# Kernel tuning notes

Measured on AMD Instinct MI355X. Metric: run time of the kernel, lower is better.

The kernel has to match this reference:

```python
import jax, jax.numpy as jnp
import numpy as np

D = 4          # simulated tensor-parallel devices (shard_axis size)
B, S = 2, 4096 # batch, seq_len
DIN_S = 512    # per-device input feature shard (full d_model = D*DIN_S = 2048)
DOUT_S = 2048  # per-device output feature shard (full d_out = D*DOUT_S = 8192)


def setup_inputs() -> dict:
    key = jax.random.key(0)
    kx, kw, kb = jax.random.split(key, 3)
    x = jax.random.normal(kx, (D, B, S, DIN_S), dtype=jnp.float32)
    # lecun_normal-style scale: std = 1/sqrt(fan_in) with fan_in = full input dim
    W = jax.random.normal(kw, (D, D, DIN_S, DOUT_S), dtype=jnp.float32) / np.sqrt(D * DIN_S)
    b = jax.random.normal(kb, (D, DOUT_S), dtype=jnp.float32) * 0.01
    return {"x": x, "W": W, "b": b}


def reference(x, W, b):
    # 'gather' TP strategy: device d gathers all input shards x_i and computes
    #   y_d = sum_i x_i @ W[d, i] + b[d]   (bias only added once, by shard idx==0)
    # x: [D, B, S, DIN_S], W: [D_out_dev, D_in_shard, DIN_S, DOUT_S], b: [D, DOUT_S]
    y = jnp.einsum('ibsk,diko->dbso', x, W)  # sum over gathered shards i and k
    return y + b[:, None, None, :]
```

## Files before the change

### kernel.cpp

```cpp
#include <hip/hip_runtime.h>
#include <hip/hip_bf16.h>

#define D_   4
#define M_   8192
#define K_   2048
#define N_   2048
#define DIN  512

typedef __attribute__((ext_vector_type(8))) short  short8v;
typedef __attribute__((ext_vector_type(4))) float  f32x4;

__device__ __forceinline__ unsigned short f2bf(float f) {
  union { float f; unsigned int u; } v; v.f = f;
  unsigned int u = v.u;
  return (unsigned short)((u + 0x7fffu + ((u >> 16) & 1u)) >> 16);
}

__global__ __launch_bounds__(256) void convert_x_kernel(const float* __restrict__ x,
                                                        unsigned short* __restrict__ A) {
  unsigned int tid = blockIdx.x * 256u + threadIdx.x;
  unsigned int kg  = tid & 63u;
  unsigned int i   = (tid >> 6) & 3u;
  unsigned int m   = tid >> 8;
  const float4* src = (const float4*)(x + (size_t)i * ((size_t)M_ * DIN)
                                        + (size_t)m * DIN + (size_t)kg * 8);
  float4 a = src[0];
  float4 b = src[1];
  uint4 pk;
  pk.x = (unsigned int)f2bf(a.x) | ((unsigned int)f2bf(a.y) << 16);
  pk.y = (unsigned int)f2bf(a.z) | ((unsigned int)f2bf(a.w) << 16);
  pk.z = (unsigned int)f2bf(b.x) | ((unsigned int)f2bf(b.y) << 16);
  pk.w = (unsigned int)f2bf(b.z) | ((unsigned int)f2bf(b.w) << 16);
  *(uint4*)(A + (size_t)tid * 8) = pk;
}

__global__ __launch_bounds__(256) void transpose_w_kernel(const float* __restrict__ W,
                                                          unsigned short* __restrict__ Wt) {
  __shared__ float tile[64][65];
  const int d  = blockIdx.z;
  const int k0 = blockIdx.x * 64;
  const int o0 = blockIdx.y * 64;
  const int t  = threadIdx.x;
  const float* src = W + (size_t)d * ((size_t)K_ * N_) + (size_t)k0 * N_ + o0;
  const int c4 = (t & 15) * 4;
  const int r  = t >> 4;
  #pragma unroll
  for (int j = 0; j < 64; j += 16) {
    float4 v = *(const float4*)(src + (size_t)(r + j) * N_ + c4);
    tile[r + j][c4 + 0] = v.x; tile[r + j][c4 + 1] = v.y;
    tile[r + j][c4 + 2] = v.z; tile[r + j][c4 + 3] = v.w;
  }
  __syncthreads();
  unsigned short* dst = Wt + (size_t)d * ((size_t)N_ * K_);
  const int kk = (t & 7) * 8;
  const int oo = t >> 3;
  #pragma unroll
  for (int p = 0; p < 64; p += 32) {
    const int o = oo + p;
    unsigned short tmp[8];
    #pragma unroll
    for (int i = 0; i < 8; i++) tmp[i] = f2bf(tile[kk + i][o]);
    *(uint4*)(dst + (size_t)(o0 + o) * K_ + k0 + kk) = *(uint4*)tmp;
  }
}

#define GLL16(gp, lp)                                                              \
  __builtin_amdgcn_global_load_lds(                                               \
      (const __attribute__((address_space(1))) void*)(gp),                        \
      (__attribute__((address_space(3))) void*)(lp), 16, 0, 0)

__global__ __launch_bounds__(256) void gemm_kernel(const unsigned short* __restrict__ A,
                                                   const unsigned short* __restrict__ Bt,
                                                   const float* __restrict__ bias,
                                                   float* __restrict__ C) {
  __shared__ unsigned short sA[128 * 64];
  __shared__ unsigned short sB[128 * 64];
  const int tid   = threadIdx.x;
  const int wave  = tid >> 6;
  const int lane  = tid & 63;
  const int d     = blockIdx.z;

  const int lin   = blockIdx.y * 16 + blockIdx.x;
  const int xcd   = lin & 7;
  const int t     = lin >> 3;
  const int tileN = (xcd * 2 + (t & 1)) * 128;
  const int tileM = (t >> 1) * 128;

  const int srow = lane >> 3;
  const int scol = ((lane & 7) ^ srow) * 8;
  const unsigned short* gA = A + (size_t)(tileM + wave * 32 + srow) * K_ + scol;
  const unsigned short* gB = Bt + (size_t)d * ((size_t)N_ * K_)
                                + (size_t)(tileN + wave * 32 + srow) * K_ + scol;
  unsigned short* lA = sA + (wave * 32) * 64;
  unsigned short* lB = sB + (wave * 32) * 64;

  const int wm   = (wave >> 1) * 64;
  const int wn   = (wave & 1) * 64;
  const int fr   = lane & 15;
  const int qw   = lane >> 4;
  const int fc0  = (qw ^ (fr & 7)) * 8;

  f32x4 acc[4][4];
  #pragma unroll
  for (int i = 0; i < 4; i++)
    #pragma unroll
    for (int j = 0; j < 4; j++)
      acc[i][j] = (f32x4){0.f, 0.f, 0.f, 0.f};

  for (int k0 = 0; k0 < K_; k0 += 64) {
    #pragma unroll
    for (int j = 0; j < 4; j++) {
      GLL16(gA + (size_t)j * 8 * K_ + k0, lA + j * 8 * 64);
      GLL16(gB + (size_t)j * 8 * K_ + k0, lB + j * 8 * 64);
    }
    __syncthreads();

    #pragma unroll
    for (int ks = 0; ks < 2; ks++) {
      const int fc = fc0 ^ (ks * 32);
      short8v af[4], bfv[4];
      #pragma unroll
      for (int mi = 0; mi < 4; mi++)
        af[mi] = *(const short8v*)(sA + (wm + mi * 16 + fr) * 64 + fc);
      #pragma unroll
      for (int ni = 0; ni < 4; ni++)
        bfv[ni] = *(const short8v*)(sB + (wn + ni * 16 + fr) * 64 + fc);
      #pragma unroll
      for (int mi = 0; mi < 4; mi++)
        #pragma unroll
        for (int ni = 0; ni < 4; ni++)
          acc[mi][ni] = __builtin_amdgcn_mfma_f32_16x16x32_bf16(af[mi], bfv[ni],
                                                                acc[mi][ni], 0, 0, 0);
    }
    __syncthreads();
  }

  float* Cd       = C + (size_t)d * ((size_t)M_ * N_);
  const float* bd = bias + d * N_;
  #pragma unroll
  for (int ni = 0; ni < 4; ni++) {
    const int col  = tileN + wn + ni * 16 + fr;
    const float bv = bd[col];
    #pragma unroll
    for (int mi = 0; mi < 4; mi++) {
      const int row0 = tileM + wm + mi * 16 + qw * 4;
      #pragma unroll
      for (int r = 0; r < 4; r++)
        Cd[(size_t)(row0 + r) * N_ + col] = acc[mi][ni][r] + bv;
    }
  }
}

__global__ void naive_kernel(const float* __restrict__ x, const float* __restrict__ W,
                             const float* __restrict__ bias, float* __restrict__ y) {
  long idx = (long)blockIdx.x * blockDim.x + threadIdx.x;
  if (idx >= (long)D_ * M_ * N_) return;
  int  n = (int)(idx % N_);
  long t = idx / N_;
  int  m = (int)(t % M_);
  int  d = (int)(t / M_);
  float acc = bias[d * N_ + n];
  const float* wd = W + (size_t)d * ((size_t)K_ * N_);
  for (int i = 0; i < D_; i++) {
    const float* xr = x + (size_t)i * ((size_t)M_ * DIN) + (size_t)m * DIN;
    const float* wr = wd + (size_t)i * ((size_t)DIN * N_) + n;
    #pragma unroll 4
    for (int k = 0; k < DIN; k++) acc += xr[k] * wr[(size_t)k * N_];
  }
  y[idx] = acc;
}

extern "C" void kernel_launch(void* const* d_in, const int* in_sizes, int n_in,
                              void* d_out, int out_size, void* d_ws, size_t ws_size,
                              hipStream_t stream) {
  const float* x    = (const float*)d_in[0];
  const float* W    = (const float*)d_in[1];
  const float* bias = (const float*)d_in[2];
  float* out        = (float*)d_out;

  const size_t a_elems  = (size_t)M_ * K_;
  const size_t wt_elems = (size_t)D_ * N_ * K_;
  const size_t need     = (a_elems + wt_elems) * sizeof(unsigned short);

  if (ws_size >= need) {
    unsigned short* Abf = (unsigned short*)d_ws;
    unsigned short* Wt  = Abf + a_elems;

    convert_x_kernel<<<(M_ * K_ / 8) / 256, 256, 0, stream>>>(x, Abf);

    dim3 tgrid(K_ / 64, N_ / 64, D_);
    transpose_w_kernel<<<tgrid, 256, 0, stream>>>(W, Wt);

    dim3 ggrid(N_ / 128, M_ / 128, D_);
    gemm_kernel<<<ggrid, 256, 0, stream>>>(Abf, Wt, bias, out);
  } else {
    long total = (long)D_ * M_ * N_;
    naive_kernel<<<(unsigned int)((total + 255) / 256), 256, 0, stream>>>(x, W, bias, out);
  }
}
```

Before: 615.0 us.

## Use 256x256 GEMM tiles with 4-stage LDS pipeline and 512 threads

Restructures the bf16 GEMM to 256x256 block tiles with 8 waves, K-step 32, and a 4-deep ring of LDS buffers filled by direct global-to-LDS loads issued three tiles ahead. A single barrier per step with explicit vmcnt waits replaces the two-barrier load-then-compute loop, so memory latency can overlap MFMA work. It also raises MFMA priority, changes the tile-to-XCD mapping, and raises per-wave accumulator count. The cost is 128KB of LDS per block and more registers, which limits occupancy.

```diff
diff --git a/kernel.cpp b/kernel.cpp
--- a/kernel.cpp
+++ b/kernel.cpp
@@ -69,83 +69,103 @@
       (const __attribute__((address_space(1))) void*)(gp),                        \
       (__attribute__((address_space(3))) void*)(lp), 16, 0, 0)
 
-__global__ __launch_bounds__(256) void gemm_kernel(const unsigned short* __restrict__ A,
-                                                   const unsigned short* __restrict__ Bt,
-                                                   const float* __restrict__ bias,
-                                                   float* __restrict__ C) {
-  __shared__ unsigned short sA[128 * 64];
-  __shared__ unsigned short sB[128 * 64];
-  const int tid   = threadIdx.x;
-  const int wave  = tid >> 6;
-  const int lane  = tid & 63;
-  const int d     = blockIdx.z;
-
-  const int lin   = blockIdx.y * 16 + blockIdx.x;
-  const int xcd   = lin & 7;
-  const int t     = lin >> 3;
-  const int tileN = (xcd * 2 + (t & 1)) * 128;
-  const int tileM = (t >> 1) * 128;
-
-  const int srow = lane >> 3;
-  const int scol = ((lane & 7) ^ srow) * 8;
-  const unsigned short* gA = A + (size_t)(tileM + wave * 32 + srow) * K_ + scol;
-  const unsigned short* gB = Bt + (size_t)d * ((size_t)N_ * K_)
-                                + (size_t)(tileN + wave * 32 + srow) * K_ + scol;
-  unsigned short* lA = sA + (wave * 32) * 64;
-  unsigned short* lB = sB + (wave * 32) * 64;
-
-  const int wm   = (wave >> 1) * 64;
-  const int wn   = (wave & 1) * 64;
-  const int fr   = lane & 15;
-  const int qw   = lane >> 4;
-  const int fc0  = (qw ^ (fr & 7)) * 8;
-
-  f32x4 acc[4][4];
-  #pragma unroll
-  for (int i = 0; i < 4; i++)
+#define NT_ 64
+
+__global__ __launch_bounds__(512, 2) void gemm_kernel(const unsigned short* __restrict__ A,
+                                                      const unsigned short* __restrict__ Bt,
+                                                      const float* __restrict__ bias,
+                                                      float* __restrict__ C) {
+  __shared__ __align__(16) unsigned short sA[4 * 8192];
+  __shared__ __align__(16) unsigned short sB[4 * 8192];
+  const int tid  = threadIdx.x;
+  const int w    = tid >> 6;
+  const int lane = tid & 63;
+  const int d    = blockIdx.z;
+
+  const int lin     = blockIdx.y * 8 + blockIdx.x;
+  const int tile_id = (lin & 7) * 32 + (lin >> 3);
+  const int tileM   = (tile_id >> 3) * 256;
+  const int tileN   = (tile_id & 7) * 256;
+
+  const int lr = lane >> 2;
+  const int ls = lane & 3;
+  const int lc = ls ^ (lr & 3);
+  const unsigned short* gA0 = A + (size_t)(tileM + w * 32 + lr) * K_ + lc * 8;
+  const unsigned short* gA1 = gA0 + (size_t)16 * K_;
+  const unsigned short* Bd  = Bt + (size_t)d * ((size_t)N_ * K_);
+  const unsigned short* gB0 = Bd + (size_t)(tileN + w * 32 + lr) * K_ + lc * 8;
+  const unsigned short* gB1 = gB0 + (size_t)16 * K_;
+  unsigned short* lA = sA + w * 1024;
+  unsigned short* lB = sB + w * 1024;
+
+  const int wr = w >> 2;
+  const int wc = w & 3;
+  const int fr = lane & 15;
+  const int qw = lane >> 4;
+  const int frag_off = fr * 32 + ((qw ^ (fr & 3)) * 8);
+  const int aoff = wr * 4096 + frag_off;
+  const int boff = wc * 2048 + frag_off;
+
+  f32x4 acc[8][4];
+  #pragma unroll
+  for (int mi = 0; mi < 8; ++mi)
     #pragma unroll
-    for (int j = 0; j < 4; j++)
-      acc[i][j] = (f32x4){0.f, 0.f, 0.f, 0.f};
-
-  for (int k0 = 0; k0 < K_; k0 += 64) {
-    #pragma unroll
-    for (int j = 0; j < 4; j++) {
-      GLL16(gA + (size_t)j * 8 * K_ + k0, lA + j * 8 * 64);
-      GLL16(gB + (size_t)j * 8 * K_ + k0, lB + j * 8 * 64);
-    }
-    __syncthreads();
-
-    #pragma unroll
-    for (int ks = 0; ks < 2; ks++) {
-      const int fc = fc0 ^ (ks * 32);
-      short8v af[4], bfv[4];
-      #pragma unroll
-      for (int mi = 0; mi < 4; mi++)
-        af[mi] = *(const short8v*)(sA + (wm + mi * 16 + fr) * 64 + fc);
-      #pragma unroll
-      for (int ni = 0; ni < 4; ni++)
-        bfv[ni] = *(const short8v*)(sB + (wn + ni * 16 + fr) * 64 + fc);
-      #pragma unroll
-      for (int mi = 0; mi < 4; mi++)
-        #pragma unroll
-        for (int ni = 0; ni < 4; ni++)
-          acc[mi][ni] = __builtin_amdgcn_mfma_f32_16x16x32_bf16(af[mi], bfv[ni],
-                                                                acc[mi][ni], 0, 0, 0);
-    }
-    __syncthreads();
-  }
+    for (int ni = 0; ni < 4; ++ni)
+      acc[mi][ni] = (f32x4){0.f, 0.f, 0.f, 0.f};
+
+#define ISSUE_TILE(tt) do {                                                   \
+    const int    bf_ = (tt) & 3;                                              \
+    const size_t ko_ = (size_t)(tt) * 32;                                     \
+    GLL16(gA0 + ko_, lA + bf_ * 8192);                                        \
+    GLL16(gA1 + ko_, lA + bf_ * 8192 + 512);                                  \
+    GLL16(gB0 + ko_, lB + bf_ * 8192);                                        \
+    GLL16(gB1 + ko_, lB + bf_ * 8192 + 512);                                  \
+  } while (0)
+
+#define TILE_BODY(tt, WAITSTR, DOISSUE) do {                                  \
+    asm volatile(WAITSTR ::: "memory");                                       \
+    __builtin_amdgcn_s_barrier();                                             \
+    __builtin_amdgcn_sched_barrier(0);                                        \
+    if (DOISSUE) ISSUE_TILE((tt) + 3);                                        \
+    const unsigned short* bA = sA + ((tt) & 3) * 8192 + aoff;                 \
+    const unsigned short* bB = sB + ((tt) & 3) * 8192 + boff;                 \
+    short8v af[8], bfv[4];                                                    \
+    _Pragma("unroll")                                                         \
+    for (int mi = 0; mi < 8; ++mi) af[mi]  = *(const short8v*)(bA + mi * 512);\
+    _Pragma("unroll")                                                         \
+    for (int ni = 0; ni < 4; ++ni) bfv[ni] = *(const short8v*)(bB + ni * 512);\
+    __builtin_amdgcn_s_setprio(1);                                            \
+    _Pragma("unroll")                                                         \
+    for (int mi = 0; mi < 8; ++mi)                                            \
+      _Pragma("unroll")                                                       \
+      for (int ni = 0; ni < 4; ++ni)                                          \
+        acc[mi][ni] = __builtin_amdgcn_mfma_f32_16x16x32_bf16(af[mi], bfv[ni],\
+                                                              acc[mi][ni], 0, 0, 0); \
+    __builtin_amdgcn_s_setprio(0);                                            \
+  } while (0)
+
+  ISSUE_TILE(0); ISSUE_TILE(1); ISSUE_TILE(2);
+
+  for (int t = 0; t < NT_ - 2; ++t) {
+    TILE_BODY(t, "s_waitcnt vmcnt(8)", t < NT_ - 3);
+  }
+  TILE_BODY(NT_ - 2, "s_waitcnt vmcnt(4)", false);
+  TILE_BODY(NT_ - 1, "s_waitcnt vmcnt(0)", false);
+
+#undef TILE_BODY
+#undef ISSUE_TILE
 
   float* Cd       = C + (size_t)d * ((size_t)M_ * N_);
   const float* bd = bias + d * N_;
   #pragma unroll
-  for (int ni = 0; ni < 4; ni++) {
-    const int col  = tileN + wn + ni * 16 + fr;
+  for (int ni = 0; ni < 4; ++ni) {
+    const int col  = tileN + wc * 64 + ni * 16 + fr;
     const float bv = bd[col];
     #pragma unroll
-    for (int mi = 0; mi < 4; mi++) {
-      const int row0 = tileM + wm + mi * 16 + qw * 4;
+    for (int mi = 0; mi < 8; ++mi) {
+      const int row0 = tileM + wr * 128 + mi * 16 + qw * 4;
       #pragma unroll
-      for (int r = 0; r < 4; r++)
+      for (int r = 0; r < 4; ++r)
         Cd[(size_t)(row0 + r) * N_ + col] = acc[mi][ni][r] + bv;
     }
   }
@@ -191,8 +211,8 @@
     dim3 tgrid(K_ / 64, N_ / 64, D_);
     transpose_w_kernel<<<tgrid, 256, 0, stream>>>(W, Wt);
 
-    dim3 ggrid(N_ / 128, M_ / 128, D_);
-    gemm_kernel<<<ggrid, 256, 0, stream>>>(Abf, Wt, bias, out);
+    dim3 ggrid(N_ / 256, M_ / 256, D_);
+    gemm_kernel<<<ggrid, 512, 0, stream>>>(Abf, Wt, bias, out);
   } else {
     long total = (long)D_ * M_ * N_;
     naive_kernel<<<(unsigned int)((total + 255) / 256), 256, 0, stream>>>(x, W, bias, out);
```

New measurement: 668.8 us. 8.7% more time.
